# Kernel optimization log

Measured on AMD Instinct MI355X. Metric: run time of the kernel, lower is better.

The kernel has to match this reference:

```python
import jax, jax.numpy as jnp
import numpy as np

B, C, H, W = 4, 64, 64, 64

def _conv1x1(x, w, b):
    # Conv2d(k=1): y[b,o,h,w] = sum_c x[b,c,h,w]*w[o,c] + b[o]
    return jnp.einsum('bchw,oc->bohw', x, w) + b[None, :, None, None]

def setup_inputs() -> dict:
    key = jax.random.key(0)
    ks = jax.random.split(key, 8)
    s = 1.0 / np.sqrt(C)
    return {
        'v1': jax.random.normal(ks[0], (B, C, H, W), jnp.float32),
        'v2': jax.random.normal(ks[1], (B, C, H, W), jnp.float32),
        'wq': jax.random.normal(ks[2], (C, C), jnp.float32) * s,
        'bq': jax.random.normal(ks[3], (C,), jnp.float32) * 0.01,
        'wk': jax.random.normal(ks[4], (C, C), jnp.float32) * s,
        'bk': jax.random.normal(ks[5], (C,), jnp.float32) * 0.01,
        'wv': jax.random.normal(ks[6], (C, C), jnp.float32) * s,
        'bv': jax.random.normal(ks[7], (C,), jnp.float32) * 0.01,
    }

def reference(v1, v2, wq, bq, wk, bk, wv, bv):
    q = _conv1x1(v1, wq, bq)   # (B,C,H,W)
    k = _conv1x1(v2, wk, bk)
    v = _conv1x1(v2, wv, bv)
    b, c, h, w = q.shape
    n = c * h                   # tokens = C*H, feature dim = W (matches torch view)
    qf = q.reshape(b, n, w)
    kf = k.reshape(b, n, w)
    vf = v.reshape(b, n, w)
    scores = jnp.einsum('bnw,bmw->bnm', qf, kf)   # (B, N, N)
    attn = jax.nn.softmax(scores, axis=-1)
    out = jnp.einsum('bnm,bmw->bnw', attn, vf)
    return out.reshape(v1.shape)
```

## Files before the change

kernel.cpp:

```cpp
#include <hip/hip_runtime.h>


#define Bn 4
#define Cc 64
#define HW 4096
#define Nn 4096
#define Dd 64
#define TS (Bn * Nn * Dd)
#define LOG2E 1.44269504088896340736f

typedef _Float16 f16;
typedef _Float16 f16x8 __attribute__((ext_vector_type(8)));
typedef _Float16 f16x4 __attribute__((ext_vector_type(4)));
typedef __fp16 fp16x2 __attribute__((ext_vector_type(2)));
typedef float f32x4 __attribute__((ext_vector_type(4)));

__device__ __forceinline__ int swz(int row, int col) {
    return row * 64 + (col ^ ((row & 7) << 3));
}

__device__ __forceinline__ void gl_lds16(const f16* g, f16* l) {
    __builtin_amdgcn_global_load_lds(
        (const __attribute__((address_space(1))) unsigned int*)g,
        (__attribute__((address_space(3))) unsigned int*)l, 16, 0, 0);
}

__global__ __launch_bounds__(256) void qkv_conv(
    const float* __restrict__ v1, const float* __restrict__ v2,
    const float* __restrict__ wq, const float* __restrict__ bq,
    const float* __restrict__ wk, const float* __restrict__ bk,
    const float* __restrict__ wv, const float* __restrict__ bv,
    f16* __restrict__ Qh, f16* __restrict__ Kh, f16* __restrict__ Vh)
{
    const int t    = threadIdx.x;
    const int lane = t & 63;
    const int og   = __builtin_amdgcn_readfirstlane(t >> 6);
    const int b    = blockIdx.y;
    const int p    = blockIdx.x * 64 + lane;
    const int z    = blockIdx.z;
    const int zt   = z >> 1;
    const int ch0  = (z & 1) * 32 + og * 8;

    const float* w    = (zt == 0) ? wq : (zt == 1) ? wk : wv;
    const float* bias = (zt == 0) ? bq : (zt == 1) ? bk : bv;
    const float* x    = ((zt == 0) ? v1 : v2) + (size_t)b * (Cc * HW) + p;

    float acc[8];
    #pragma unroll
    for (int j = 0; j < 8; ++j) acc[j] = bias[ch0 + j];
    #pragma unroll 16
    for (int c = 0; c < 64; ++c) {
        float xc = x[c * HW];
        #pragma unroll
        for (int j = 0; j < 8; ++j)
            acc[j] = fmaf(w[(ch0 + j) * 64 + c], xc, acc[j]);
    }

    f16* dst = (zt == 0) ? Qh : (zt == 1) ? Kh : Vh;
    const float scale = (zt == 0) ? LOG2E : 1.0f;
    #pragma unroll
    for (int j = 0; j < 8; ++j) {
        size_t idx = (size_t)b * (Nn * Dd) + (size_t)(ch0 + j) * 4096 + p;
        dst[idx] = (f16)(acc[j] * scale);
    }
}

__global__ __launch_bounds__(256) void vtrans(const f16* __restrict__ Vh,
                                              f16* __restrict__ Vt)
{
    __shared__ f16 tile[64][72];
    const int t  = threadIdx.x;
    const int n0 = blockIdx.x * 64;
    const int b  = blockIdx.y;
    for (int i = t; i < 4096; i += 256) {
        int r = i >> 6, c = i & 63;
        tile[r][c] = Vh[(size_t)b * (Nn * Dd) + (size_t)(n0 + r) * 64 + c];
    }
    __syncthreads();
    for (int i = t; i < 4096; i += 256) {
        int w = i >> 6, n = i & 63;
        Vt[(size_t)b * (Dd * Nn) + (size_t)w * Nn + n0 + n] = tile[n][w];
    }
}

__global__ __launch_bounds__(512, 4) void attn(
    const f16* __restrict__ Qhg, const f16* __restrict__ Khg,
    const f16* __restrict__ Vtg,
    float* __restrict__ out, f16* __restrict__ Opart, float2* __restrict__ ml)
{
    __shared__ __align__(16) f16 KT[2][4096];
    __shared__ __align__(16) f16 VT[2][4096];
    __shared__ __align__(16) f16 Pt[16384];

    const int t    = threadIdx.x;
    const int lane = t & 63, wvi = t >> 6;
    const int g = lane >> 4, c = lane & 15;
    const int b  = blockIdx.z;
    const int sp = blockIdx.y;
    const int S  = gridDim.y;
    const int n0 = blockIdx.x * 256;
    const int keysPerSplit = Nn / S;
    const int nTiles = keysPerSplit / 64;
    const int kbase = sp * keysPerSplit;

    const int srow = t >> 3;
    const int gc   = ((t & 7) ^ (srow & 7)) * 8;
    f16* ldsKdst0 = &KT[0][(wvi * 8) * 64];
    f16* ldsKdst1 = &KT[1][(wvi * 8) * 64];
    f16* ldsVdst0 = &VT[0][(wvi * 8) * 64];
    f16* ldsVdst1 = &VT[1][(wvi * 8) * 64];

    const f16* Kb = Khg + (size_t)b * (Nn * Dd);
    const f16* Vb = Vtg + (size_t)b * (Dd * Nn);

    f16x8 qbh[2][2];
    #pragma unroll
    for (int qf = 0; qf < 2; ++qf) {
        const int qrow = n0 + wvi * 32 + qf * 16 + c;
        const f16* qhp = Qhg + ((size_t)b * Nn + qrow) * 64;
        #pragma unroll
        for (int ks = 0; ks < 2; ++ks)
            qbh[qf][ks] = *(const f16x8*)(qhp + ks * 32 + g * 8);
    }

    float m_run[2] = {-1e30f, -1e30f}, lpart[2] = {0.f, 0.f};
    f32x4 of[2][4];
    #pragma unroll
    for (int qf = 0; qf < 2; ++qf)
        #pragma unroll
        for (int nf = 0; nf < 4; ++nf)
            #pragma unroll
            for (int r = 0; r < 4; ++r) of[qf][nf][r] = 0.f;

    gl_lds16(Kb + (size_t)(kbase + srow) * 64 + gc, ldsKdst0);
    gl_lds16(Vb + (size_t)srow * Nn + kbase + gc, ldsVdst0);
    __syncthreads();
    int cur = 0;

    for (int kt = 0; kt < nTiles; ++kt) {
        if (kt + 1 < nTiles) {
            const int k0n = kbase + (kt + 1) * 64;
            f16* kd = cur ? ldsKdst0 : ldsKdst1;
            f16* vd = cur ? ldsVdst0 : ldsVdst1;
            gl_lds16(Kb + (size_t)(k0n + srow) * 64 + gc, kd);
            gl_lds16(Vb + (size_t)srow * Nn + k0n + gc, vd);
        }

        const f16* KTc = KT[cur];
        const f16* VTc = VT[cur];

        f32x4 accS[2][4];
        #pragma unroll
        for (int qf = 0; qf < 2; ++qf)
            #pragma unroll
            for (int fm = 0; fm < 4; ++fm)
                #pragma unroll
                for (int r = 0; r < 4; ++r) accS[qf][fm][r] = 0.f;
        #pragma unroll
        for (int fm = 0; fm < 4; ++fm) {
            const int key = fm * 16 + c;
            f16x8 kh0 = *(const f16x8*)(KTc + swz(key, g * 8));
            f16x8 kh1 = *(const f16x8*)(KTc + swz(key, 32 + g * 8));
            #pragma unroll
            for (int qf = 0; qf < 2; ++qf) {
                accS[qf][fm] = __builtin_amdgcn_mfma_f32_16x16x32_f16(kh0, qbh[qf][0], accS[qf][fm], 0, 0, 0);
                accS[qf][fm] = __builtin_amdgcn_mfma_f32_16x16x32_f16(kh1, qbh[qf][1], accS[qf][fm], 0, 0, 0);
            }
        }

        #pragma unroll
        for (int qf = 0; qf < 2; ++qf) {
            float m0 = fmaxf(fmaxf(accS[qf][0][0], accS[qf][0][1]),
                             fmaxf(accS[qf][0][2], accS[qf][0][3]));
            float m1 = fmaxf(fmaxf(accS[qf][1][0], accS[qf][1][1]),
                             fmaxf(accS[qf][1][2], accS[qf][1][3]));
            float m2 = fmaxf(fmaxf(accS[qf][2][0], accS[qf][2][1]),
                             fmaxf(accS[qf][2][2], accS[qf][2][3]));
            float m3 = fmaxf(fmaxf(accS[qf][3][0], accS[qf][3][1]),
                             fmaxf(accS[qf][3][2], accS[qf][3][3]));
            float tmax = fmaxf(fmaxf(m0, m1), fmaxf(m2, m3));
            tmax = fmaxf(tmax, __shfl_xor(tmax, 16));
            tmax = fmaxf(tmax, __shfl_xor(tmax, 32));
            if (!__all(tmax <= m_run[qf] + 8.f)) {
                const float mnew = fmaxf(m_run[qf], tmax);
                const float corr = exp2f(m_run[qf] - mnew);
                lpart[qf] *= corr;
                #pragma unroll
                for (int r = 0; r < 4; ++r) {
                    float cr = __shfl(corr, g * 4 + r);
                    #pragma unroll
                    for (int nf = 0; nf < 4; ++nf) of[qf][nf][r] *= cr;
                }
                m_run[qf] = mnew;
            }
            float s01 = 0.f, s23 = 0.f;
            #pragma unroll
            for (int fm = 0; fm < 4; ++fm)
                #pragma unroll
                for (int r = 0; r < 4; ++r) {
                    float pp = exp2f(accS[qf][fm][r] - m_run[qf]);
                    accS[qf][fm][r] = pp;
                    if (fm < 2) s01 += pp; else s23 += pp;
                }
            lpart[qf] += s01 + s23;

            const int prow = wvi * 32 + qf * 16 + c;
            #pragma unroll
            for (int fm = 0; fm < 4; ++fm) {
                union { f16x4 v4; fp16x2 h2[2]; } u;
                u.h2[0] = __builtin_amdgcn_cvt_pkrtz(accS[qf][fm][0], accS[qf][fm][1]);
                u.h2[1] = __builtin_amdgcn_cvt_pkrtz(accS[qf][fm][2], accS[qf][fm][3]);
                *(f16x4*)(Pt + swz(prow, fm * 16 + g * 4)) = u.v4;
            }
        }

        #pragma unroll
        for (int ks = 0; ks < 2; ++ks) {
            f16x8 pa0 = *(const f16x8*)(Pt + swz(wvi * 32 + c,      ks * 32 + g * 8));
            f16x8 pa1 = *(const f16x8*)(Pt + swz(wvi * 32 + 16 + c, ks * 32 + g * 8));
            #pragma unroll
            for (int nf = 0; nf < 4; ++nf) {
                f16x8 vb = *(const f16x8*)(VTc + swz(nf * 16 + c, ks * 32 + g * 8));
                of[0][nf] = __builtin_amdgcn_mfma_f32_16x16x32_f16(pa0, vb, of[0][nf], 0, 0, 0);
                of[1][nf] = __builtin_amdgcn_mfma_f32_16x16x32_f16(pa1, vb, of[1][nf], 0, 0, 0);
            }
        }

        __syncthreads();
        cur ^= 1;
    }

    if (S == 1) {
        #pragma unroll
        for (int qf = 0; qf < 2; ++qf) {
            float lr = lpart[qf];
            lr += __shfl_xor(lr, 16);
            lr += __shfl_xor(lr, 32);
            const float linv = 1.0f / lr;
            #pragma unroll
            for (int r = 0; r < 4; ++r) {
                float li = __shfl(linv, g * 4 + r);
                int n = n0 + wvi * 32 + qf * 16 + g * 4 + r;
                #pragma unroll
                for (int nf = 0; nf < 4; ++nf)
                    out[((size_t)b * Nn + n) * 64 + nf * 16 + c] = of[qf][nf][r] * li;
            }
        }
    } else {
        #pragma unroll
        for (int qf = 0; qf < 2; ++qf) {
            float lr = lpart[qf];
            lr += __shfl_xor(lr, 16);
            lr += __shfl_xor(lr, 32);
            const float linv = 1.0f / lr;
            #pragma unroll
            for (int r = 0; r < 4; ++r) {
                float li = __shfl(linv, g * 4 + r);
                int n = n0 + wvi * 32 + qf * 16 + g * 4 + r;
                size_t robase = (((size_t)sp * Bn + b) * Nn + n) * 64;
                #pragma unroll
                for (int nf = 0; nf < 4; ++nf)
                    Opart[robase + nf * 16 + c] = (f16)(of[qf][nf][r] * li);
            }
            if (lane < 16) {
                int n = n0 + wvi * 32 + qf * 16 + c;
                ml[((size_t)sp * Bn + b) * Nn + n] = make_float2(m_run[qf], lr);
            }
        }
    }
}

__global__ __launch_bounds__(256) void combine(
    const f16* __restrict__ Opart, const float2* __restrict__ ml,
    float* __restrict__ out, int S)
{
    const int idx8 = blockIdx.x * 256 + threadIdx.x;
    const int w8 = idx8 & 7;
    const int n  = (idx8 >> 3) & (Nn - 1);
    const int b  = idx8 >> 15;
    float M = -1e30f;
    for (int s = 0; s < S; ++s)
        M = fmaxf(M, ml[((size_t)s * Bn + b) * Nn + n].x);
    float num[8];
    #pragma unroll
    for (int j = 0; j < 8; ++j) num[j] = 0.f;
    float den = 0.f;
    for (int s = 0; s < S; ++s) {
        float2 m2 = ml[((size_t)s * Bn + b) * Nn + n];
        float a = exp2f(m2.x - M) * m2.y;
        f16x8 o8 = *(const f16x8*)(Opart + ((((size_t)s * Bn + b) * Nn + n) << 6) + w8 * 8);
        #pragma unroll
        for (int j = 0; j < 8; ++j) num[j] += a * (float)o8[j];
        den += a;
    }
    const float di = 1.0f / den;
    float* op = out + (((size_t)b * Nn + n) << 6) + w8 * 8;
    float4 lo = make_float4(num[0] * di, num[1] * di, num[2] * di, num[3] * di);
    float4 hi = make_float4(num[4] * di, num[5] * di, num[6] * di, num[7] * di);
    *(float4*)op = lo;
    *(float4*)(op + 4) = hi;
}

extern "C" void kernel_launch(void* const* d_in, const int* in_sizes, int n_in,
                              void* d_out, int out_size, void* d_ws, size_t ws_size,
                              hipStream_t stream)
{
    const float* v1 = (const float*)d_in[0];
    const float* v2 = (const float*)d_in[1];
    const float* wq = (const float*)d_in[2];
    const float* bq = (const float*)d_in[3];
    const float* wk = (const float*)d_in[4];
    const float* bk = (const float*)d_in[5];
    const float* wv = (const float*)d_in[6];
    const float* bv = (const float*)d_in[7];
    float* out = (float*)d_out;

    char* ws = (char*)d_ws;
    const size_t T = (size_t)TS * sizeof(f16);
    f16* Qh = (f16*)(ws + 0 * T);
    f16* Kh = (f16*)(ws + 1 * T);
    f16* Vh = (f16*)(ws + 2 * T);
    f16* Vt = (f16*)(ws + 3 * T);
    const size_t base = 4 * T;
    const size_t opartBytes = (size_t)TS * 2;
    const size_t mlBytes    = (size_t)Bn * Nn * 8;

    int S = 1;
    if      (ws_size >= base + 8 * (opartBytes + mlBytes)) S = 8;
    else if (ws_size >= base + 4 * (opartBytes + mlBytes)) S = 4;
    else if (ws_size >= base + 2 * (opartBytes + mlBytes)) S = 2;

    f16*    Opart = (f16*)(ws + base);
    float2* mlp   = (float2*)(ws + base + (size_t)S * opartBytes);

    qkv_conv<<<dim3(64, 4, 6), 256, 0, stream>>>(v1, v2, wq, bq, wk, bk, wv, bv,
                                                 Qh, Kh, Vh);
    vtrans<<<dim3(64, 4), 256, 0, stream>>>(Vh, Vt);
    attn<<<dim3(16, S, 4), 512, 0, stream>>>(Qh, Kh, Vt, out, Opart, mlp);
    if (S > 1) {
        combine<<<(Bn * Nn * Dd / 8) / 256, 256, 0, stream>>>(Opart, mlp, out, S);
    }
}
```

Baseline: 69.62 us.

## Keep softmax probabilities in registers for PV MFMA, dropping LDS staging

```diff
diff --git a/kernel.cpp b/kernel.cpp
--- a/kernel.cpp
+++ b/kernel.cpp
@@ -83,14 +83,13 @@
     }
 }
 
-__global__ __launch_bounds__(512, 4) void attn(
+__global__ __launch_bounds__(512, 8) void attn(
     const f16* __restrict__ Qhg, const f16* __restrict__ Khg,
     const f16* __restrict__ Vtg,
     float* __restrict__ out, f16* __restrict__ Opart, float2* __restrict__ ml)
 {
     __shared__ __align__(16) f16 KT[2][4096];
     __shared__ __align__(16) f16 VT[2][4096];
-    __shared__ __align__(16) f16 Pt[16384];
 
     const int t    = threadIdx.x;
     const int lane = t & 63, wvi = t >> 6;
@@ -168,6 +167,7 @@
             }
         }
 
+        f16x4 pb[2][4];
         #pragma unroll
         for (int qf = 0; qf < 2; ++qf) {
             float m0 = fmaxf(fmaxf(accS[qf][0][0], accS[qf][0][1]),
@@ -186,43 +186,35 @@
                 const float corr = exp2f(m_run[qf] - mnew);
                 lpart[qf] *= corr;
                 #pragma unroll
-                for (int r = 0; r < 4; ++r) {
-                    float cr = __shfl(corr, g * 4 + r);
+                for (int nf = 0; nf < 4; ++nf)
                     #pragma unroll
-                    for (int nf = 0; nf < 4; ++nf) of[qf][nf][r] *= cr;
-                }
+                    for (int r = 0; r < 4; ++r) of[qf][nf][r] *= corr;
                 m_run[qf] = mnew;
             }
             float s01 = 0.f, s23 = 0.f;
             #pragma unroll
-            for (int fm = 0; fm < 4; ++fm)
+            for (int fm = 0; fm < 4; ++fm) {
                 #pragma unroll
                 for (int r = 0; r < 4; ++r) {
                     float pp = exp2f(accS[qf][fm][r] - m_run[qf]);
                     accS[qf][fm][r] = pp;
                     if (fm < 2) s01 += pp; else s23 += pp;
                 }
-            lpart[qf] += s01 + s23;
-
-            const int prow = wvi * 32 + qf * 16 + c;
-            #pragma unroll
-            for (int fm = 0; fm < 4; ++fm) {
                 union { f16x4 v4; fp16x2 h2[2]; } u;
                 u.h2[0] = __builtin_amdgcn_cvt_pkrtz(accS[qf][fm][0], accS[qf][fm][1]);
                 u.h2[1] = __builtin_amdgcn_cvt_pkrtz(accS[qf][fm][2], accS[qf][fm][3]);
-                *(f16x4*)(Pt + swz(prow, fm * 16 + g * 4)) = u.v4;
-            }
-        }
-
-        #pragma unroll
-        for (int ks = 0; ks < 2; ++ks) {
-            f16x8 pa0 = *(const f16x8*)(Pt + swz(wvi * 32 + c,      ks * 32 + g * 8));
-            f16x8 pa1 = *(const f16x8*)(Pt + swz(wvi * 32 + 16 + c, ks * 32 + g * 8));
-            #pragma unroll
-            for (int nf = 0; nf < 4; ++nf) {
-                f16x8 vb = *(const f16x8*)(VTc + swz(nf * 16 + c, ks * 32 + g * 8));
-                of[0][nf] = __builtin_amdgcn_mfma_f32_16x16x32_f16(pa0, vb, of[0][nf], 0, 0, 0);
-                of[1][nf] = __builtin_amdgcn_mfma_f32_16x16x32_f16(pa1, vb, of[1][nf], 0, 0, 0);
+                pb[qf][fm] = u.v4;
+            }
+            lpart[qf] += s01 + s23;
+        }
+
+        #pragma unroll
+        for (int nf = 0; nf < 4; ++nf) {
+            #pragma unroll
+            for (int fm = 0; fm < 4; ++fm) {
+                f16x4 va = *(const f16x4*)(VTc + swz(nf * 16 + c, fm * 16 + g * 4));
+                of[0][nf] = __builtin_amdgcn_mfma_f32_16x16x16f16(va, pb[0][fm], of[0][nf], 0, 0, 0);
+                of[1][nf] = __builtin_amdgcn_mfma_f32_16x16x16f16(va, pb[1][fm], of[1][nf], 0, 0, 0);
             }
         }
 
@@ -237,13 +229,12 @@
             lr += __shfl_xor(lr, 16);
             lr += __shfl_xor(lr, 32);
             const float linv = 1.0f / lr;
-            #pragma unroll
-            for (int r = 0; r < 4; ++r) {
-                float li = __shfl(linv, g * 4 + r);
-                int n = n0 + wvi * 32 + qf * 16 + g * 4 + r;
-                #pragma unroll
-                for (int nf = 0; nf < 4; ++nf)
-                    out[((size_t)b * Nn + n) * 64 + nf * 16 + c] = of[qf][nf][r] * li;
+            const int n = n0 + wvi * 32 + qf * 16 + c;
+            #pragma unroll
+            for (int nf = 0; nf < 4; ++nf) {
+                float4 o4 = make_float4(of[qf][nf][0] * linv, of[qf][nf][1] * linv,
+                                        of[qf][nf][2] * linv, of[qf][nf][3] * linv);
+                *(float4*)(out + (((size_t)b * Nn + n) << 6) + nf * 16 + g * 4) = o4;
             }
         }
     } else {
@@ -253,17 +244,16 @@
             lr += __shfl_xor(lr, 16);
             lr += __shfl_xor(lr, 32);
             const float linv = 1.0f / lr;
-            #pragma unroll
-            for (int r = 0; r < 4; ++r) {
-                float li = __shfl(linv, g * 4 + r);
-                int n = n0 + wvi * 32 + qf * 16 + g * 4 + r;
-                size_t robase = (((size_t)sp * Bn + b) * Nn + n) * 64;
-                #pragma unroll
-                for (int nf = 0; nf < 4; ++nf)
-                    Opart[robase + nf * 16 + c] = (f16)(of[qf][nf][r] * li);
-            }
-            if (lane < 16) {
-                int n = n0 + wvi * 32 + qf * 16 + c;
+            const int n = n0 + wvi * 32 + qf * 16 + c;
+            size_t robase = (((size_t)sp * Bn + b) * Nn + n) << 6;
+            #pragma unroll
+            for (int nf = 0; nf < 4; ++nf) {
+                union { f16x4 v4; fp16x2 h2[2]; } u;
+                u.h2[0] = __builtin_amdgcn_cvt_pkrtz(of[qf][nf][0] * linv, of[qf][nf][1] * linv);
+                u.h2[1] = __builtin_amdgcn_cvt_pkrtz(of[qf][nf][2] * linv, of[qf][nf][3] * linv);
+                *(f16x4*)(Opart + robase + nf * 16 + g * 4) = u.v4;
+            }
+            if (g == 0) {
                 ml[((size_t)sp * Bn + b) * Nn + n] = make_float2(m_run[qf], lr);
             }
         }
@@ -326,9 +316,10 @@
     const size_t mlBytes    = (size_t)Bn * Nn * 8;
 
     int S = 1;
-    if      (ws_size >= base + 8 * (opartBytes + mlBytes)) S = 8;
-    else if (ws_size >= base + 4 * (opartBytes + mlBytes)) S = 4;
-    else if (ws_size >= base + 2 * (opartBytes + mlBytes)) S = 2;
+    if      (ws_size >= base + 16 * (opartBytes + mlBytes)) S = 16;
+    else if (ws_size >= base +  8 * (opartBytes + mlBytes)) S = 8;
+    else if (ws_size >= base +  4 * (opartBytes + mlBytes)) S = 4;
+    else if (ws_size >= base +  2 * (opartBytes + mlBytes)) S = 2;
 
     f16*    Opart = (f16*)(ws + base);
     float2* mlp   = (float2*)(ws + base + (size_t)S * opartBytes);
```

After: 229.7 us. 230% more time.
